# Kernel tuning notes

Measured on AMD Instinct MI355X. Metric: run time of the kernel, lower is better.

Reference implementation:

```python
import jax, jax.numpy as jnp
import numpy as np
from jax import lax

SHIFTS = (1, 2, 4, 8)

def _neighbors(x, d):
    # x: [B,C,H,W] -> [B,8,C,H,W], 8 reflection-padded directional shifts
    H, W = x.shape[2], x.shape[3]
    def p(t, l, b, r):
        return jnp.pad(x, ((0, 0), (0, 0), (t, b), (l, r)), mode='reflect')
    x0 = p(d, d, 0, 0)[:, :, :H, :W]
    x1 = p(d, 0, 0, 0)[:, :, :H, :]
    x2 = p(d, 0, 0, d)[:, :, :H, d:]
    x3 = p(0, d, 0, 0)[:, :, :, :W]
    x4 = p(0, 0, 0, d)[:, :, :, d:]
    x5 = p(0, d, d, 0)[:, :, d:, :W]
    x6 = p(0, 0, d, 0)[:, :, d:, :]
    x7 = p(0, 0, d, d)[:, :, d:, d:]
    return jnp.stack([x0, x1, x2, x3, x4, x5, x6, x7], axis=1)

def _l2norm(x):
    # F.normalize(dim=-1): x / max(||x||, 1e-12)
    n = jnp.sqrt(jnp.sum(x * x, axis=-1, keepdims=True))
    return x / jnp.maximum(n, 1e-12)

def _forward(cen, q_w, k_w, v_w, sur_w1, sur_b1, sur_w2, sur_b2, sum_weights, out_w, bn_gamma, bn_beta):
    B, C, H, W = cen.shape
    nh = len(SHIFTS)
    keys, qrys, vals = [], [], []
    for i, d in enumerate(SHIFTS):
        nb = _neighbors(cen, d)  # [B,8,C,H,W]
        w2 = jax.nn.softmax(sum_weights[i])  # [2]
        h1 = lax.conv_general_dilated(cen, sur_w1[i], (1, 1), ((d, d), (d, d)),
                                      rhs_dilation=(d, d),
                                      dimension_numbers=('NCHW', 'OIHW', 'NCHW'))
        h1 = jax.nn.relu(h1 + sur_b1[i][None, :, None, None])
        sw = jax.nn.softmax(jnp.einsum('bchw,oc->bohw', h1, sur_w2[i]) + sur_b2[i][None, :, None, None], axis=1) * w2[0]  # [B,8,H,W]
        sum_x = jnp.einsum('bkchw,bkhw->bchw', nb, sw) + cen * w2[1]
        cen_x = nb.mean(axis=1) * w2[0] + cen * w2[1]
        sur = (nb - sum_x[:, None]).reshape(B, 8 * C, H, W)  # cat of x_k - sum_x
        keys.append(jnp.einsum('bchw,oc->bohw', sur, k_w[i]))    # [B,8*hid,H,W]
        vals.append(jnp.einsum('bchw,oc->bohw', sur, v_w[i]))
        qrys.append(jnp.einsum('bchw,oc->bohw', cen_x, q_w[i]))  # [B,hid,H,W]
    HW = H * W
    # torch.stack(dim=2).view(b, nh, -1, HW): row-major reinterpretation
    K = jnp.stack(keys, axis=2).reshape(B, nh, -1, HW)
    Q = jnp.stack(qrys, axis=2).reshape(B, nh, -1, HW)
    V = jnp.stack(vals, axis=2).reshape(B, nh, -1, HW)
    K = _l2norm(K)
    Q = _l2norm(Q)
    score = jnp.einsum('bnqs,bnks->bnqk', Q, K) / np.float32(np.sqrt(HW))
    # InstanceNorm2d(nh), affine=False: normalize over last two dims per (b, head)
    mu = score.mean(axis=(-2, -1), keepdims=True)
    var = score.var(axis=(-2, -1), keepdims=True)
    score = (score - mu) * lax.rsqrt(var + 1e-5)
    attn = jax.nn.softmax(score, axis=-1)
    out = jnp.einsum('bnqk,bnks->bnqs', attn, V).reshape(B, -1, H, W)  # [B,tra,H,W]
    y = jnp.einsum('bchw,oc->bohw', out, out_w)
    # BatchNorm2d in training mode (batch statistics)
    m = y.mean(axis=(0, 2, 3), keepdims=True)
    v = y.var(axis=(0, 2, 3), keepdims=True)
    y = (y - m) * lax.rsqrt(v + 1e-5) * bn_gamma[None, :, None, None] + bn_beta[None, :, None, None]
    return jax.nn.relu(y)

def setup_inputs() -> dict:
    key = jax.random.key(0)
    ks = jax.random.split(key, 12)
    B, C, H, W = 2, 32, 128, 128
    nh, hid, tra, oc = 4, 64, 256, 256
    r = lambda k, s, sc: jax.random.normal(k, s, dtype=jnp.float32) * sc
    return {
        'cen': r(ks[0], (B, C, H, W), 1.0),
        'q_w': r(ks[1], (nh, hid, C), 0.05),
        'k_w': r(ks[2], (nh, 8 * hid, 8 * C), 0.05),
        'v_w': r(ks[3], (nh, 8 * hid, 8 * C), 0.05),
        'sur_w1': r(ks[4], (nh, C, C, 3, 3), 0.05),
        'sur_b1': r(ks[5], (nh, C), 0.02),
        'sur_w2': r(ks[6], (nh, 8, C), 0.05),
        'sur_b2': r(ks[7], (nh, 8), 0.02),
        'sum_weights': r(ks[8], (nh, 2), 0.1),
        'out_w': r(ks[9], (oc, tra), 0.05),
        'bn_gamma': jnp.ones((oc,), jnp.float32) + r(ks[10], (oc,), 0.05),
        'bn_beta': r(ks[11], (oc,), 0.05),
    }

def reference(cen, q_w, k_w, v_w, sur_w1, sur_b1, sur_w2, sur_b2, sum_weights, out_w, bn_gamma, bn_beta):
    return _forward(cen, q_w, k_w, v_w, sur_w1, sur_b1, sur_w2, sur_b2, sum_weights, out_w, bn_gamma, bn_beta)
```

## Files before the change

### kernel.cpp

```cpp
#include <hip/hip_runtime.h>


#define HW 16384
typedef unsigned short u16;
typedef unsigned int u32;
typedef __attribute__((ext_vector_type(8))) short short8;
typedef __attribute__((ext_vector_type(4))) float f32x4;

#define S_CEN 0
#define S_QW 1048576
#define S_KW 1056768
#define S_VW 1581056
#define S_W1 2105344
#define S_B1 2142208
#define S_W2 2142336
#define S_B2 2143360
#define S_SW 2143392
#define S_OW 2143400
#define S_GAMMA 2208936
#define S_BETA 2209192
#define S_TOTAL 2209456

#define G_D1 0
#define G_D2 16384
#define G_S 147456
#define G_SZ 409600

#define GP_SLOT 344064

__device__ __forceinline__ float b2f(u16 u) { return __uint_as_float(((u32)u) << 16); }
__device__ __forceinline__ u16 f2b(float f) {
  u32 u = __float_as_uint(f);
  return (u16)((u + 0x7FFFu + ((u >> 16) & 1u)) >> 16);
}
__device__ __forceinline__ float wave_sum(float v) {
  #pragma unroll
  for (int off = 32; off > 0; off >>= 1) v += __shfl_xor(v, off, 64);
  return v;
}
__device__ __forceinline__ float wave_max(float v) {
  #pragma unroll
  for (int off = 32; off > 0; off >>= 1) v = fmaxf(v, __shfl_xor(v, off, 64));
  return v;
}
__device__ __forceinline__ void unpack8(uint4 v, float* f) {
  f[0] = __uint_as_float(v.x << 16); f[1] = __uint_as_float(v.x & 0xFFFF0000u);
  f[2] = __uint_as_float(v.y << 16); f[3] = __uint_as_float(v.y & 0xFFFF0000u);
  f[4] = __uint_as_float(v.z << 16); f[5] = __uint_as_float(v.z & 0xFFFF0000u);
  f[6] = __uint_as_float(v.w << 16); f[7] = __uint_as_float(v.w & 0xFFFF0000u);
}
__device__ __forceinline__ void gload16(const u16* g, u16* l) {
  __builtin_amdgcn_global_load_lds(
      (const __attribute__((address_space(1))) void*)g,
      (__attribute__((address_space(3))) void*)l, 16, 0, 0);
}

__device__ __forceinline__ void tile_decode(int tile, int& r0, int& c0,
                                            size_t& goff, int& gstride) {
  if (tile == 0) { r0 = 0; c0 = 0; goff = G_D1; gstride = 128; }
  else if (tile < 9) { r0 = 0; c0 = 128 * tile; goff = G_D2 + (size_t)(tile - 1) * 128; gstride = 1024; }
  else if (tile < 17) {
    int t2 = tile - 9; int j = t2 >> 1, p = t2 & 1;
    r0 = 128 + 256 * j + 128 * p; c0 = r0;
    goff = G_S + (size_t)j * 65536 + (size_t)p * (128 * 256 + 128); gstride = 256;
  } else {
    int j = tile - 17;
    r0 = 128 + 256 * j; c0 = r0 + 128;
    goff = G_S + (size_t)j * 65536 + 128; gstride = 256;
  }
}

__global__ void probe(const u32* __restrict__ g, int* __restrict__ flag) {
  if (threadIdx.x == 0) {
    int ok = 1;
    #pragma unroll
    for (int i = 0; i < 4; i++) {
      u32 w = g[i];
      u32 lo = w & 0xFFFFu, hi = w >> 16;
      ok &= (lo >= 0x3E00u && lo <= 0x4100u) ? 1 : 0;
      ok &= (hi >= 0x3E00u && hi <= 0x4100u) ? 1 : 0;
    }
    *flag = ok ? 0 : 1;
  }
}

__global__ __launch_bounds__(256) void convert_all(
    const void* p0, const void* p1, const void* p2, const void* p3,
    const void* p4, const void* p5, const void* p6, const void* p7,
    const void* p8, const void* p9, const void* p10, const void* p11,
    u16* __restrict__ S, const int* __restrict__ flag) {
  const void* src; int n; int off;
  switch (blockIdx.z) {
    case 0:  src = p0;  n = 1048576; off = S_CEN; break;
    case 1:  src = p1;  n = 8192;    off = S_QW; break;
    case 2:  src = p2;  n = 524288;  off = S_KW; break;
    case 3:  src = p3;  n = 524288;  off = S_VW; break;
    case 4:  src = p4;  n = 36864;   off = S_W1; break;
    case 5:  src = p5;  n = 128;     off = S_B1; break;
    case 6:  src = p6;  n = 1024;    off = S_W2; break;
    case 7:  src = p7;  n = 32;      off = S_B2; break;
    case 8:  src = p8;  n = 8;       off = S_SW; break;
    case 9:  src = p9;  n = 65536;   off = S_OW; break;
    case 10: src = p10; n = 256;     off = S_GAMMA; break;
    default: src = p11; n = 256;     off = S_BETA; break;
  }
  int idx = (blockIdx.x * 256 + threadIdx.x) * 4;
  if (idx >= n) return;
  u16* dst = S + off + idx;
  if (*flag) {
    float4 v = ((const float4*)src)[idx >> 2];
    dst[0] = f2b(v.x); dst[1] = f2b(v.y); dst[2] = f2b(v.z); dst[3] = f2b(v.w);
  } else {
    *(ushort4*)dst = ((const ushort4*)src)[idx >> 2];
  }
}

__global__ __launch_bounds__(256) void sur_w(
    const u16* __restrict__ cen, const u16* __restrict__ w1g,
    const u16* __restrict__ b1g, const u16* __restrict__ w2g,
    float* __restrict__ lgbuf) {
  const int z = blockIdx.y;
  const int b = z >> 2, si = z & 3, d = 1 << si;
  __shared__ float w1s[9][32][32];
  __shared__ float w2s[8][32];
  __shared__ float b1s[32];
  const int t = threadIdx.x;
  for (int e = t; e < 9216; e += 256) {
    int tap = e >> 10, rem = e & 1023, ci = rem >> 5, co = rem & 31;
    w1s[tap][ci][co] = b2f(w1g[si * 9216 + co * 288 + ci * 9 + tap]);
  }
  w2s[t >> 5][t & 31] = b2f(w2g[si * 256 + t]);
  if (t < 32) b1s[t] = b2f(b1g[si * 32 + t]);
  __syncthreads();

  const int px = t >> 1;
  const int half = t & 1;
  const int ch = half * 16;
  const int hh = blockIdx.x;
  const int s = hh * 128 + px;
  const u16* cb = cen + (size_t)b * 32 * HW + (size_t)ch * HW;

  float h1[32];
  #pragma unroll
  for (int i = 0; i < 32; i++) h1[i] = 0.f;
  for (int tap = 0; tap < 9; tap++) {
    int ky = tap / 3, kx = tap - ky * 3;
    int y = hh + (ky - 1) * d, x = px + (kx - 1) * d;
    bool valid = (y >= 0 && y < 128 && x >= 0 && x < 128);
    int yc = y < 0 ? 0 : (y > 127 ? 127 : y);
    int xc = x < 0 ? 0 : (x > 127 ? 127 : x);
    int off = yc * 128 + xc;
    float vb[16];
    #pragma unroll
    for (int ci = 0; ci < 16; ci++) vb[ci] = b2f(cb[(size_t)ci * HW + off]);
    #pragma unroll
    for (int ci = 0; ci < 16; ci++) {
      float v = valid ? vb[ci] : 0.f;
      #pragma unroll
      for (int i = 0; i < 32; i++) h1[i] = fmaf(v, w1s[tap][ch + ci][i], h1[i]);
    }
  }
  #pragma unroll
  for (int i = 0; i < 32; i++) h1[i] += __shfl_xor(h1[i], 1, 64);
  #pragma unroll
  for (int i = 0; i < 32; i++) h1[i] = fmaxf(h1[i] + b1s[i], 0.f);

  float lp[4];
  #pragma unroll
  for (int k = 0; k < 4; k++) lp[k] = 0.f;
  #pragma unroll
  for (int i = 0; i < 32; i++) {
    float v = h1[i];
    #pragma unroll
    for (int k = 0; k < 4; k++) lp[k] = fmaf(v, w2s[half * 4 + k][i], lp[k]);
  }
  float* dst = lgbuf + ((size_t)z * HW + s) * 8 + half * 4;
  *(float4*)dst = make_float4(lp[0], lp[1], lp[2], lp[3]);
}

__global__ __launch_bounds__(256) void sur_scatter(
    const u16* __restrict__ cen, const float* __restrict__ lgbuf,
    const u16* __restrict__ b2g, const u16* __restrict__ swg,
    u16* __restrict__ Mbuf) {
  const int z = blockIdx.z;
  const int b = z >> 2, si = z & 3, d = 1 << si;
  const int c0 = blockIdx.y * 8;
  const int t = threadIdx.x;
  const int s = (blockIdx.x * 256 + t) * 2;
  const int h = s >> 7, w = s & 127;

  float s0 = b2f(swg[si * 2 + 0]), s1 = b2f(swg[si * 2 + 1]);
  float mx = fmaxf(s0, s1);
  float e0 = expf(s0 - mx), e1 = expf(s1 - mx);
  float w20 = e0 / (e0 + e1), w21 = e1 / (e0 + e1);

  float b2s[8];
  #pragma unroll
  for (int k = 0; k < 8; k++) b2s[k] = b2f(b2g[si * 8 + k]);

  const float* lpa = lgbuf + ((size_t)z * HW + s) * 8;
  float lga[8], lgb[8];
  {
    float4 a0 = *(const float4*)lpa,       a1 = *(const float4*)(lpa + 4);
    float4 g0 = *(const float4*)(lpa + 8), g1 = *(const float4*)(lpa + 12);
    lga[0] = a0.x; lga[1] = a0.y; lga[2] = a0.z; lga[3] = a0.w;
    lga[4] = a1.x; lga[5] = a1.y; lga[6] = a1.z; lga[7] = a1.w;
    lgb[0] = g0.x; lgb[1] = g0.y; lgb[2] = g0.z; lgb[3] = g0.w;
    lgb[4] = g1.x; lgb[5] = g1.y; lgb[6] = g1.z; lgb[7] = g1.w;
  }
  {
    #pragma unroll
    for (int k = 0; k < 8; k++) lga[k] += b2s[k];
    float lm = lga[0];
    #pragma unroll
    for (int k = 1; k < 8; k++) lm = fmaxf(lm, lga[k]);
    float ls = 0.f;
    #pragma unroll
    for (int k = 0; k < 8; k++) { lga[k] = expf(lga[k] - lm); ls += lga[k]; }
    float inv = w20 / ls;
    #pragma unroll
    for (int k = 0; k < 8; k++) lga[k] *= inv;
  }
  {
    #pragma unroll
    for (int k = 0; k < 8; k++) lgb[k] += b2s[k];
    float lm = lgb[0];
    #pragma unroll
    for (int k = 1; k < 8; k++) lm = fmaxf(lm, lgb[k]);
    float ls = 0.f;
    #pragma unroll
    for (int k = 0; k < 8; k++) { lgb[k] = expf(lgb[k] - lm); ls += lgb[k]; }
    float inv = w20 / ls;
    #pragma unroll
    for (int k = 0; k < 8; k++) lgb[k] *= inv;
  }

  const int dy[8] = {-d, -d, -d, 0, 0, d, d, d};
  const int dx[8] = {-d, 0, d, -d, d, -d, 0, d};
  int offa[8], offb[8];
  #pragma unroll
  for (int k = 0; k < 8; k++) {
    int y = h + dy[k]; y = y < 0 ? -y : (y > 127 ? 254 - y : y);
    int xa = w + dx[k]; xa = xa < 0 ? -xa : (xa > 127 ? 254 - xa : xa);
    int xb = w + 1 + dx[k]; xb = xb < 0 ? -xb : (xb > 127 ? 254 - xb : xb);
    offa[k] = y * 128 + xa;
    offb[k] = y * 128 + xb;
  }
  const u16* cb = cen + (size_t)b * 32 * HW;
  u16* Mb = Mbuf + (size_t)b * 1152 * HW;
  for (int c = c0; c < c0 + 8; c++) {
    const u16* cc = cb + (size_t)c * HW;
    u32 cvp = *(const u32*)&cc[s];
    float cva = __uint_as_float(cvp << 16), cvb = __uint_as_float(cvp & 0xFFFF0000u);
    float nba[8], nbb[8];
    #pragma unroll
    for (int k = 0; k < 8; k++) { nba[k] = b2f(cc[offa[k]]); nbb[k] = b2f(cc[offb[k]]); }
    float sxa = 0.f, mna = 0.f, sxb = 0.f, mnb = 0.f;
    #pragma unroll
    for (int k = 0; k < 8; k++) {
      sxa = fmaf(lga[k], nba[k], sxa); mna += nba[k];
      sxb = fmaf(lgb[k], nbb[k], sxb); mnb += nbb[k];
    }
    float suma = sxa + cva * w21, sumb = sxb + cvb * w21;
    u32 cx = (u32)f2b(mna * 0.125f * w20 + cva * w21) |
             ((u32)f2b(mnb * 0.125f * w20 + cvb * w21) << 16);
    *(u32*)&Mb[(size_t)(32 * si + c) * HW + s] = cx;
    #pragma unroll
    for (int k = 0; k < 8; k++) {
      u32 pk = (u32)f2b(nba[k] - suma) | ((u32)f2b(nbb[k] - sumb) << 16);
      *(u32*)&Mb[(size_t)(128 + 256 * si + k * 32 + c) * HW + s] = pk;
    }
  }
}

__global__ __launch_bounds__(256) void gram_mfma(
    const u16* __restrict__ Mbuf, float* __restrict__ Gpart) {
  const int id = blockIdx.x;
  const int tile = id >> 5, combo = id & 31;
  const int ks = combo >> 1, b = combo & 1;
  int r0, c0, gstride; size_t goff;
  tile_decode(tile, r0, c0, goff, gstride);
  const bool diag = (r0 == c0);
  const u16* Mb = Mbuf + (size_t)b * 1152 * HW;
  __shared__ u16 As[128 * 64];
  __shared__ u16 Bs[128 * 64];
  const int t = threadIdx.x;
  const int lane = t & 63, w = t >> 6;
  const int wr = w >> 1, wc = w & 1;
  const int m = lane & 15, quad = lane >> 4;
  const int lr = lane >> 3;
  const int lsl = ((lane & 7) ^ (lr & 7)) * 8;
  const int kbase = ks * 1024;
  f32x4 acc[4][4];
  #pragma unroll
  for (int i = 0; i < 4; i++)
    #pragma unroll
    for (int j = 0; j < 4; j++) acc[i][j] = (f32x4){0.f, 0.f, 0.f, 0.f};

  for (int s0 = kbase; s0 < kbase + 1024; s0 += 64) {
    #pragma unroll
    for (int q = 0; q < 4; q++) {
      const int R0 = w * 32 + q * 8;
      gload16(Mb + (size_t)(r0 + R0 + lr) * HW + s0 + lsl, &As[R0 * 64]);
    }
    if (!diag) {
      #pragma unroll
      for (int q = 0; q < 4; q++) {
        const int R0 = w * 32 + q * 8;
        gload16(Mb + (size_t)(c0 + R0 + lr) * HW + s0 + lsl, &Bs[R0 * 64]);
      }
    }
    __syncthreads();
    const u16* Bb = diag ? As : Bs;
    #pragma unroll
    for (int kh = 0; kh < 2; kh++) {
      short8 af[4], bf[4];
      const int slot = ((quad + 4 * kh) ^ (m & 7)) * 8;
      #pragma unroll
      for (int i = 0; i < 4; i++)
        af[i] = *(const short8*)&As[(wr * 64 + i * 16 + m) * 64 + slot];
      #pragma unroll
      for (int j = 0; j < 4; j++)
        bf[j] = *(const short8*)&Bb[(wc * 64 + j * 16 + m) * 64 + slot];
      #pragma unroll
      for (int i = 0; i < 4; i++)
        #pragma unroll
        for (int j = 0; j < 4; j++)
          acc[i][j] = __builtin_amdgcn_mfma_f32_16x16x32_bf16(af[i], bf[j], acc[i][j], 0, 0, 0);
    }
    __syncthreads();
  }
  float* Gb = Gpart + (size_t)(b * 16 + ks) * GP_SLOT + (size_t)tile * 16384;
  #pragma unroll
  for (int i = 0; i < 4; i++)
    #pragma unroll
    for (int j = 0; j < 4; j++) {
      int col = wc * 64 + j * 16 + m;
      #pragma unroll
      for (int r = 0; r < 4; r++) {
        int row = wr * 64 + i * 16 + quad * 4 + r;
        Gb[row * 128 + col] = acc[i][j][r];
      }
    }
}

__global__ __launch_bounds__(256) void greduce(
    const float* __restrict__ Gpart, float* __restrict__ G) {
  const int chunk = blockIdx.x, tile = blockIdx.y, b = blockIdx.z;
  int r0, c0, gstride; size_t goff;
  tile_decode(tile, r0, c0, goff, gstride);
  const int t = threadIdx.x;
  const int e = chunk * 1024 + t * 4;
  const float* base = Gpart + (size_t)b * 16 * GP_SLOT + (size_t)tile * 16384 + e;
  f32x4 acc = *(const f32x4*)base;
  #pragma unroll
  for (int s = 1; s < 16; s++) acc += *(const f32x4*)(base + (size_t)s * GP_SLOT);
  const int row = e >> 7, col = e & 127;
  *(f32x4*)&G[(size_t)b * G_SZ + goff + (size_t)row * gstride + col] = acc;
}

__global__ __launch_bounds__(256) void mirror_S(float* __restrict__ G) {
  const int j = blockIdx.x & 3, b = blockIdx.x >> 2;
  float* base = G + (size_t)b * G_SZ + G_S + (size_t)j * 65536;
  const int t = threadIdx.x;
  for (int e = t; e < 16384; e += 256) {
    int rr = e >> 7, cc = e & 127;
    base[(size_t)(128 + rr) * 256 + cc] = base[(size_t)cc * 256 + 128 + rr];
  }
}

__global__ __launch_bounds__(64) void qnorm(
    const u16* __restrict__ qw, const float* __restrict__ G,
    float* __restrict__ invQ) {
  const int bn = blockIdx.x, b = bn >> 2, n = bn & 3;
  const int rq = threadIdx.x;
  const int i = rq & 3, q1r = rq >> 2;
  const u16* qr = qw + ((size_t)(i * 64) + 16 * n + q1r) * 32;
  float v[32];
  #pragma unroll
  for (int c = 0; c < 32; c++) v[c] = b2f(qr[c]);
  const float* D1 = G + (size_t)b * G_SZ;
  float ss = 0.f;
  for (int c = 0; c < 32; c++) {
    float tmp = 0.f;
    #pragma unroll
    for (int c2 = 0; c2 < 32; c2++) tmp = fmaf(v[c2], D1[(size_t)(32 * i + c2) * 128 + 32 * i + c], tmp);
    ss = fmaf(tmp, v[c], ss);
  }
  invQ[bn * 64 + rq] = 1.f / fmaxf(sqrtf(fmaxf(ss, 0.f)), 1e-12f);
}

__global__ __launch_bounds__(256) void knorm(
    const u16* __restrict__ kw, const float* __restrict__ G,
    float* __restrict__ invK) {
  const int jj = blockIdx.x;
  const int j = jj & 3, kkg = jj >> 2;
  const int n = blockIdx.y, b = blockIdx.z;
  const int t = threadIdx.x;
  __shared__ float vs[8][256];
  for (int e = t; e < 2048; e += 256) {
    int r = e >> 8, c = e & 255;
    vs[r][c] = b2f(kw[((size_t)(j * 512) + 128 * n + kkg * 8 + r) * 256 + c]);
  }
  __syncthreads();
  const float* S = G + (size_t)b * G_SZ + G_S + (size_t)j * 65536;
  float acc[8];
  #pragma unroll
  for (int r = 0; r < 8; r++) acc[r] = 0.f;
  for (int c2 = 0; c2 < 256; c2++) {
    float sv = S[(size_t)c2 * 256 + t];
    #pragma unroll
    for (int r = 0; r < 8; r++) acc[r] = fmaf(vs[r][c2], sv, acc[r]);
  }
  #pragma unroll
  for (int r = 0; r < 8; r++) acc[r] *= vs[r][t];
  __shared__ float red[8][4];
  const int wv = t >> 6, lane = t & 63;
  #pragma unroll
  for (int r = 0; r < 8; r++) {
    float v = wave_sum(acc[r]);
    if (lane == 0) red[r][wv] = v;
  }
  __syncthreads();
  if (t < 8) {
    float tot = fmaxf(red[t][0] + red[t][1] + red[t][2] + red[t][3], 0.f);
    invK[(size_t)(b * 4 + n) * 512 + 4 * (kkg * 8 + t) + j] =
        1.f / fmaxf(sqrtf(tot), 1e-12f);
  }
}

__global__ __launch_bounds__(256) void score2(
    const u16* __restrict__ qw, const u16* __restrict__ kw,
    const float* __restrict__ G, const float* __restrict__ invQ,
    const float* __restrict__ invK, float* __restrict__ score,
    float* __restrict__ sstat) {
  const int jj = blockIdx.x;
  const int j = jj >> 1, half = jj & 1;
  const int n = blockIdx.y, b = blockIdx.z;
  const float* D2 = G + (size_t)b * G_SZ + G_D2;
  const u16* kwb = kw + ((size_t)(j * 512) + 128 * n + half * 64) * 256;
  __shared__ float As[64][132];
  __shared__ u16 Bs[64][68];
  __shared__ float KD[128][68];
  __shared__ float qws[64][32];
  const int t = threadIdx.x;
  const int tx = t & 7, ty = t >> 3;
  float acc[4][8];
  #pragma unroll
  for (int i = 0; i < 4; i++)
    #pragma unroll
    for (int u = 0; u < 8; u++) acc[i][u] = 0.f;
  for (int ch0 = 0; ch0 < 256; ch0 += 64) {
    for (int e = t; e < 8192; e += 256) {
      int r = e >> 6, kc = e & 63;
      As[kc][r] = D2[(size_t)r * 1024 + j * 256 + ch0 + kc];
    }
    for (int e = t; e < 4096; e += 256) {
      int r = e >> 6, kc = e & 63;
      Bs[kc][r] = kwb[(size_t)r * 256 + ch0 + kc];
    }
    __syncthreads();
    #pragma unroll 4
    for (int kc = 0; kc < 64; kc++) {
      float a[4];
      #pragma unroll
      for (int i = 0; i < 4; i++) a[i] = As[kc][ty * 4 + i];
      float bb[8];
      #pragma unroll
      for (int u = 0; u < 8; u++) bb[u] = b2f(Bs[kc][tx * 8 + u]);
      #pragma unroll
      for (int i = 0; i < 4; i++)
        #pragma unroll
        for (int u = 0; u < 8; u++) acc[i][u] = fmaf(a[i], bb[u], acc[i][u]);
    }
    __syncthreads();
  }
  #pragma unroll
  for (int i = 0; i < 4; i++)
    #pragma unroll
    for (int u = 0; u < 8; u++) KD[ty * 4 + i][tx * 8 + u] = acc[i][u];
  for (int e = t; e < 2048; e += 256) {
    int q = e >> 5, c = e & 31;
    int i = q & 3, q1r = q >> 2;
    qws[q][c] = b2f(qw[((size_t)(i * 64) + 16 * n + q1r) * 32 + c]);
  }
  __syncthreads();
  const int bn = b * 4 + n;
  float* sb = score + (size_t)bn * 64 * 512;
  const float* iQ = invQ + bn * 64;
  const float* iK = invK + (size_t)bn * 512;
  const float isc = 1.f / 128.f;
  float lsum = 0.f, lss = 0.f;
  for (int e = t; e < 4096; e += 256) {
    int q = e >> 6, kkl = e & 63;
    int i = q & 3;
    float s = 0.f;
    #pragma unroll
    for (int c = 0; c < 32; c++) s = fmaf(qws[q][c], KD[i * 32 + c][kkl], s);
    int col = 4 * (half * 64 + kkl) + j;
    float v = s * iQ[q] * iK[col] * isc;
    sb[(size_t)q * 512 + col] = v;
    lsum += v; lss += v * v;
  }
  lsum = wave_sum(lsum); lss = wave_sum(lss);
  __shared__ float redp[8];
  if ((t & 63) == 0) { redp[t >> 6] = lsum; redp[4 + (t >> 6)] = lss; }
  __syncthreads();
  if (t == 0) {
    atomicAdd(&sstat[bn * 2],     redp[0] + redp[1] + redp[2] + redp[3]);
    atomicAdd(&sstat[bn * 2 + 1], redp[4] + redp[5] + redp[6] + redp[7]);
  }
}

__global__ __launch_bounds__(256) void in_softmax(
    float* __restrict__ score, const float* __restrict__ sstat) {
  const int bn = blockIdx.y, rg = blockIdx.x;
  float* sb = score + (size_t)bn * 64 * 512;
  const int t = threadIdx.x;
  float mean = sstat[bn * 2] * (1.f / 32768.f);
  float var = sstat[bn * 2 + 1] * (1.f / 32768.f) - mean * mean;
  float istd = rsqrtf(var + 1e-5f);
  const int wv = t >> 6, lane = t & 63;
  for (int rr = wv; rr < 8; rr += 4) {
    int r = rg * 8 + rr;
    float z[8];
    float m = -1e30f;
    #pragma unroll
    for (int jx = 0; jx < 8; jx++) {
      z[jx] = (sb[(size_t)r * 512 + lane + 64 * jx] - mean) * istd;
      m = fmaxf(m, z[jx]);
    }
    m = wave_max(m);
    float sloc = 0.f;
    #pragma unroll
    for (int jx = 0; jx < 8; jx++) { z[jx] = expf(z[jx] - m); sloc += z[jx]; }
    sloc = wave_sum(sloc);
    float rinv = 1.f / sloc;
    #pragma unroll
    for (int jx = 0; jx < 8; jx++) sb[(size_t)r * 512 + lane + 64 * jx] = z[jx] * rinv;
  }
}

__global__ __launch_bounds__(256) void attnW2(
    const float* __restrict__ attn, const u16* __restrict__ vw,
    float* __restrict__ W2) {
  const int j = blockIdx.x >> 2, n = blockIdx.x & 3;
  const int q0 = blockIdx.y * 8, b = blockIdx.z, bn = b * 4 + n;
  const float* ab = attn + (size_t)bn * 64 * 512;
  const int t = threadIdx.x;
  __shared__ float at_s[8][128];
  for (int e = t; e < 1024; e += 256) {
    int qg = e >> 7, kk = e & 127;
    at_s[qg][kk] = ab[(size_t)(q0 + qg) * 512 + 4 * kk + j];
  }
  __syncthreads();
  float acc[8];
  #pragma unroll
  for (int qg = 0; qg < 8; qg++) acc[qg] = 0.f;
  const u16* vcol = vw + ((size_t)(j * 512) + 128 * n) * 256 + t;
  for (int kk = 0; kk < 128; kk++) {
    float v = b2f(vcol[(size_t)kk * 256]);
    #pragma unroll
    for (int qg = 0; qg < 8; qg++) acc[qg] = fmaf(at_s[qg][kk], v, acc[qg]);
  }
  #pragma unroll
  for (int qg = 0; qg < 8; qg++)
    W2[((size_t)bn * 64 + q0 + qg) * 1024 + j * 256 + t] = acc[qg];
}

__global__ __launch_bounds__(256) void wfin_k(
    const u16* __restrict__ ow, const float* __restrict__ W2,
    u16* __restrict__ Wfin16) {
  const int jc = blockIdx.x, b = blockIdx.y;
  __shared__ float col[256];
  const int t = threadIdx.x;
  col[t] = W2[((size_t)b * 256 + t) * 1024 + jc];
  __syncthreads();
  float acc = 0.f;
  const u16* owr = ow + (size_t)t * 256;
  for (int c = 0; c < 256; c++) acc = fmaf(b2f(owr[c]), col[c], acc);
  Wfin16[((size_t)b * 256 + t) * 1024 + jc] = f2b(acc);
}

__global__ __launch_bounds__(256) void y_gemm_mfma(
    const u16* __restrict__ Wfin16, const u16* __restrict__ Mbuf,
    u16* __restrict__ ybuf) {
  const int b = blockIdx.y, col0 = blockIdx.x * 64;
  __shared__ u16 As[2][256 * 64];
  __shared__ u16 Bs[2][64 * 64];
  const u16* Ab = Wfin16 + (size_t)b * 256 * 1024;
  const u16* Mb = Mbuf + (size_t)b * 1152 * HW + (size_t)128 * HW;
  const int t = threadIdx.x;
  const int lane = t & 63, w = t >> 6;
  const int m = lane & 15, quad = lane >> 4;
  const int kp = t >> 3, cs = t & 7;
  const int lr = lane >> 3;
  const int lsl = ((lane & 7) ^ (lr & 7)) * 8;
  f32x4 acc[4][4];
  #pragma unroll
  for (int i = 0; i < 4; i++)
    #pragma unroll
    for (int j = 0; j < 4; j++) acc[i][j] = (f32x4){0.f, 0.f, 0.f, 0.f};

  uint4 v0, v1;
  auto stageA = [&](int buf, int k0c) {
    #pragma unroll
    for (int q = 0; q < 8; q++)
      gload16(&Ab[(size_t)(w * 64 + q * 8 + lr) * 1024 + k0c + lsl],
              &As[buf][(w * 64 + q * 8) * 64]);
  };
  auto loadB = [&](int k0c) {
    v0 = *(const uint4*)&Mb[(size_t)(k0c + 2 * kp) * HW + col0 + cs * 8];
    v1 = *(const uint4*)&Mb[(size_t)(k0c + 2 * kp + 1) * HW + col0 + cs * 8];
  };
  auto writeB = [&](int buf) {
    u16 t0[8], t1[8];
    *(uint4*)t0 = v0; *(uint4*)t1 = v1;
    const int ksl = kp >> 2, kin = (2 * kp) & 7;
    #pragma unroll
    for (int uu = 0; uu < 8; uu++) {
      int u = (uu + t) & 7;
      int r = cs * 8 + u;
      u32 pair = (u32)t0[u] | ((u32)t1[u] << 16);
      *(u32*)&Bs[buf][r * 64 + ((ksl ^ (r & 7)) << 3) + kin] = pair;
    }
  };

  stageA(0, 0);
  loadB(0);
  writeB(0);
  __syncthreads();

  int cur = 0;
  for (int step = 0; step < 16; step++) {
    const int nxt = cur ^ 1;
    if (step < 15) {
      stageA(nxt, (step + 1) * 64);
      loadB((step + 1) * 64);
    }
    #pragma unroll
    for (int kh = 0; kh < 2; kh++) {
      short8 af[4], bf[4];
      const int slot = ((4 * kh + quad) ^ (m & 7)) * 8;
      #pragma unroll
      for (int i = 0; i < 4; i++)
        af[i] = *(const short8*)&As[cur][(w * 64 + i * 16 + m) * 64 + slot];
      #pragma unroll
      for (int j = 0; j < 4; j++)
        bf[j] = *(const short8*)&Bs[cur][(j * 16 + m) * 64 + slot];
      #pragma unroll
      for (int i = 0; i < 4; i++)
        #pragma unroll
        for (int j = 0; j < 4; j++)
          acc[i][j] = __builtin_amdgcn_mfma_f32_16x16x32_bf16(af[i], bf[j], acc[i][j], 0, 0, 0);
    }
    if (step < 15) {
      writeB(nxt);
      __syncthreads();
      cur = nxt;
    }
  }
  #pragma unroll
  for (int i = 0; i < 4; i++)
    #pragma unroll
    for (int j = 0; j < 4; j++) {
      int col = col0 + j * 16 + m;
      #pragma unroll
      for (int r = 0; r < 4; r++) {
        int row = w * 64 + i * 16 + quad * 4 + r;
        ybuf[((size_t)b * 256 + row) * HW + col] = f2b(acc[i][j][r]);
      }
    }
}

__global__ __launch_bounds__(256) void bn_stats(
    const u16* __restrict__ y, float* __restrict__ st) {
  const int o = blockIdx.x;
  const int t = threadIdx.x;
  float sum = 0.f, ss = 0.f;
  for (int bb = 0; bb < 2; bb++) {
    const u16* p = y + ((size_t)bb * 256 + o) * HW;
    for (int e = t; e < HW / 8; e += 256) {
      uint4 v = ((const uint4*)p)[e];
      float f[8];
      unpack8(v, f);
      #pragma unroll
      for (int k = 0; k < 8; k++) { sum += f[k]; ss += f[k] * f[k]; }
    }
  }
  __shared__ float red[8];
  sum = wave_sum(sum); ss = wave_sum(ss);
  if ((t & 63) == 0) { red[t >> 6] = sum; red[4 + (t >> 6)] = ss; }
  __syncthreads();
  if (t == 0) {
    float mean = (red[0] + red[1] + red[2] + red[3]) / 32768.f;
    float var = (red[4] + red[5] + red[6] + red[7]) / 32768.f - mean * mean;
    st[o * 2] = mean;
    st[o * 2 + 1] = rsqrtf(var + 1e-5f);
  }
}

__global__ __launch_bounds__(256) void bn_apply(
    const u16* __restrict__ y, const float* __restrict__ st,
    const u16* __restrict__ gamma, const u16* __restrict__ beta,
    const int* __restrict__ flag, void* __restrict__ out) {
  const int idx8 = blockIdx.x * 256 + threadIdx.x;
  const int r = idx8 >> 11;
  const int o = r & 255;
  float mean = st[o * 2], istd = st[o * 2 + 1];
  float g = b2f(gamma[o]), be = b2f(beta[o]);
  uint4 v = ((const uint4*)y)[idx8];
  float f[8];
  unpack8(v, f);
  float rr[8];
  #pragma unroll
  for (int k = 0; k < 8; k++) rr[k] = fmaxf((f[k] - mean) * istd * g + be, 0.f);
  if (*flag) {
    float* of = (float*)out + (size_t)idx8 * 8;
    *(float4*)of = make_float4(rr[0], rr[1], rr[2], rr[3]);
    *(float4*)(of + 4) = make_float4(rr[4], rr[5], rr[6], rr[7]);
  } else {
    u32 p0 = (u32)f2b(rr[0]) | ((u32)f2b(rr[1]) << 16);
    u32 p1 = (u32)f2b(rr[2]) | ((u32)f2b(rr[3]) << 16);
    u32 p2 = (u32)f2b(rr[4]) | ((u32)f2b(rr[5]) << 16);
    u32 p3 = (u32)f2b(rr[6]) | ((u32)f2b(rr[7]) << 16);
    ((uint4*)out)[idx8] = make_uint4(p0, p1, p2, p3);
  }
}

extern "C" void kernel_launch(void* const* d_in, const int* in_sizes, int n_in,
                              void* d_out, int out_size, void* d_ws, size_t ws_size,
                              hipStream_t stream) {
  float* G     = (float*)d_ws;
  float* score = G + 819200;
  float* invQ  = score + 262144;
  float* invK  = invQ + 512;
  float* W2    = invK + 4096;
  float* Wfin  = W2 + 524288;
  float* bnst  = Wfin + 524288;
  float* sstat = bnst + 512;
  int* flag    = (int*)(sstat + 16);
  u16* Sbuf    = (u16*)(flag + 16);
  u16* Mbuf    = Sbuf + S_TOTAL;
  u16* ybuf    = Mbuf + 37748736;
  u16* Wfin16  = (u16*)Wfin;
  float* lgbuf = (float*)ybuf;
  float* Gpart = (float*)ybuf;

  probe<<<1, 64, 0, stream>>>((const u32*)d_in[10], flag);
  convert_all<<<dim3(1024, 1, 12), 256, 0, stream>>>(
      d_in[0], d_in[1], d_in[2], d_in[3], d_in[4], d_in[5], d_in[6], d_in[7],
      d_in[8], d_in[9], d_in[10], d_in[11], Sbuf, flag);

  sur_w<<<dim3(128, 8), 256, 0, stream>>>(
      Sbuf + S_CEN, Sbuf + S_W1, Sbuf + S_B1, Sbuf + S_W2, lgbuf);
  sur_scatter<<<dim3(32, 4, 8), 256, 0, stream>>>(
      Sbuf + S_CEN, lgbuf, Sbuf + S_B2, Sbuf + S_SW, Mbuf);
  hipMemsetAsync(sstat, 0, 16 * sizeof(float), stream);
  gram_mfma<<<672, 256, 0, stream>>>(Mbuf, Gpart);
  greduce<<<dim3(16, 21, 2), 256, 0, stream>>>(Gpart, G);
  mirror_S<<<8, 256, 0, stream>>>(G);
  qnorm<<<8, 64, 0, stream>>>(Sbuf + S_QW, G, invQ);
  knorm<<<dim3(64, 4, 2), 256, 0, stream>>>(Sbuf + S_KW, G, invK);
  score2<<<dim3(8, 4, 2), 256, 0, stream>>>(
      Sbuf + S_QW, Sbuf + S_KW, G, invQ, invK, score, sstat);
  in_softmax<<<dim3(8, 8), 256, 0, stream>>>(score, sstat);
  attnW2<<<dim3(16, 8, 2), 256, 0, stream>>>(score, Sbuf + S_VW, W2);
  wfin_k<<<dim3(1024, 2), 256, 0, stream>>>(Sbuf + S_OW, W2, Wfin16);
  y_gemm_mfma<<<dim3(256, 2), 256, 0, stream>>>(Wfin16, Mbuf, ybuf);
  bn_stats<<<256, 256, 0, stream>>>(ybuf, bnst);
  bn_apply<<<4096, 256, 0, stream>>>(ybuf, bnst, Sbuf + S_GAMMA, Sbuf + S_BETA,
                                     flag, d_out);
}
```

Measured before the change: 425.0 us.

## Compute dilated 3x3 surround conv with bf16 MFMA on channel-last transposed input

Adds a transpose kernel that writes cen in pixel-major, channel-last layout, then rewrites sur_w to stage each tap's input rows into shared memory and run the 32x32 per-tap products with 16x16x32 bf16 MFMA instead of scalar FMAs. Weights stay bf16 in a swizzled shared layout. Out-of-range taps are skipped per row, or read zeros from a zero buffer per pixel. h1 is staged through shared memory for the final 8-way projection. This removes a large scalar FMA loop and strided per-channel global loads, at the cost of an extra kernel launch, a transpose pass and more barriers.

```diff
diff --git a/kernel.cpp b/kernel.cpp
--- a/kernel.cpp
+++ b/kernel.cpp
@@ -115,66 +115,115 @@
   }
 }
 
+__global__ __launch_bounds__(256) void transp(
+    const u16* __restrict__ cen, u16* __restrict__ cenT) {
+  __shared__ u16 tile[32][258];
+  const int t = threadIdx.x;
+  const int s0 = blockIdx.x * 256;
+  const u16* cb = cen + (size_t)blockIdx.y * 32 * HW;
+  for (int e = t; e < 2048; e += 256) {
+    int ci = e >> 6, sx = (e & 63) * 4;
+    *(u32*)&tile[ci][sx] = *(const u32*)&cb[(size_t)ci * HW + s0 + sx];
+    *(u32*)&tile[ci][sx + 2] = *(const u32*)&cb[(size_t)ci * HW + s0 + sx + 2];
+  }
+  __syncthreads();
+  u16* ob = cenT + (size_t)blockIdx.y * HW * 32;
+  for (int e = t; e < 1024; e += 256) {
+    int px = e >> 2, cg = (e & 3) * 8;
+    u16 tmp[8];
+    #pragma unroll
+    for (int k = 0; k < 8; k++) tmp[k] = tile[cg + k][px];
+    *(uint4*)&ob[(size_t)(s0 + px) * 32 + cg] = *(uint4*)tmp;
+  }
+}
+
 __global__ __launch_bounds__(256) void sur_w(
-    const u16* __restrict__ cen, const u16* __restrict__ w1g,
+    const u16* __restrict__ cenT, const u16* __restrict__ w1g,
     const u16* __restrict__ b1g, const u16* __restrict__ w2g,
-    float* __restrict__ lgbuf) {
+    const u16* __restrict__ zbuf, float* __restrict__ lgbuf) {
   const int z = blockIdx.y;
   const int b = z >> 2, si = z & 3, d = 1 << si;
-  __shared__ float w1s[9][32][32];
+  const int hh = blockIdx.x;
+  __shared__ __align__(16) char smem[27776];
+  u16* Bs = (u16*)smem;
+  u16* w1s = (u16*)(smem + 8192);
+  float* h1s = (float*)smem;
   __shared__ float w2s[8][32];
   __shared__ float b1s[32];
   const int t = threadIdx.x;
   for (int e = t; e < 9216; e += 256) {
-    int tap = e >> 10, rem = e & 1023, ci = rem >> 5, co = rem & 31;
-    w1s[tap][ci][co] = b2f(w1g[si * 9216 + co * 288 + ci * 9 + tap]);
+    int tap = e >> 10, rem = e & 1023, co = rem >> 5, ci = rem & 31;
+    int dst = tap * 1024 + co * 32 + ((((ci >> 3) ^ (co & 3)) << 3) | (ci & 7));
+    w1s[dst] = w1g[si * 9216 + co * 288 + ci * 9 + tap];
   }
   w2s[t >> 5][t & 31] = b2f(w2g[si * 256 + t]);
   if (t < 32) b1s[t] = b2f(b1g[si * 32 + t]);
-  __syncthreads();
-
-  const int px = t >> 1;
-  const int half = t & 1;
-  const int ch = half * 16;
-  const int hh = blockIdx.x;
-  const int s = hh * 128 + px;
-  const u16* cb = cen + (size_t)b * 32 * HW + (size_t)ch * HW;
-
-  float h1[32];
-  #pragma unroll
-  for (int i = 0; i < 32; i++) h1[i] = 0.f;
+
+  const u16* cb = cenT + (size_t)b * HW * 32;
+  const int lane = t & 63, w = t >> 6;
+  const int m = lane & 15, quad = lane >> 4;
+  const int slot8 = (quad ^ (m & 3)) << 3;
+  f32x4 acc[2][2];
+  #pragma unroll
+  for (int i = 0; i < 2; i++)
+    #pragma unroll
+    for (int j = 0; j < 2; j++) acc[i][j] = (f32x4){0.f, 0.f, 0.f, 0.f};
+
   for (int tap = 0; tap < 9; tap++) {
-    int ky = tap / 3, kx = tap - ky * 3;
-    int y = hh + (ky - 1) * d, x = px + (kx - 1) * d;
-    bool valid = (y >= 0 && y < 128 && x >= 0 && x < 128);
-    int yc = y < 0 ? 0 : (y > 127 ? 127 : y);
-    int xc = x < 0 ? 0 : (x > 127 ? 127 : x);
-    int off = yc * 128 + xc;
-    float vb[16];
-    #pragma unroll
-    for (int ci = 0; ci < 16; ci++) vb[ci] = b2f(cb[(size_t)ci * HW + off]);
-    #pragma unroll
-    for (int ci = 0; ci < 16; ci++) {
-      float v = valid ? vb[ci] : 0.f;
-      #pragma unroll
-      for (int i = 0; i < 32; i++) h1[i] = fmaf(v, w1s[tap][ch + ci][i], h1[i]);
-    }
-  }
-  #pragma unroll
-  for (int i = 0; i < 32; i++) h1[i] += __shfl_xor(h1[i], 1, 64);
-  #pragma unroll
-  for (int i = 0; i < 32; i++) h1[i] = fmaxf(h1[i] + b1s[i], 0.f);
-
+    const int ky = tap / 3, kx = tap - ky * 3;
+    const int y = hh + (ky - 1) * d;
+    if (y < 0 || y > 127) continue;
+    const int dx = (kx - 1) * d;
+    #pragma unroll
+    for (int q = 0; q < 2; q++) {
+      const int e = q * 256 + t;
+      const int px = e >> 2, ck = e & 3;
+      const int x = px + dx;
+      const u16* src = ((unsigned)x < 128u)
+          ? cb + ((size_t)(y * 128 + x) * 32 + ((ck ^ (px & 3)) << 3))
+          : zbuf;
+      gload16(src, Bs + (size_t)e * 8);
+    }
+    __syncthreads();
+    short8 af[2], bf[2];
+    #pragma unroll
+    for (int i = 0; i < 2; i++)
+      af[i] = *(const short8*)&Bs[(w * 32 + i * 16 + m) * 32 + slot8];
+    #pragma unroll
+    for (int j = 0; j < 2; j++)
+      bf[j] = *(const short8*)&w1s[tap * 1024 + (j * 16 + m) * 32 + slot8];
+    #pragma unroll
+    for (int i = 0; i < 2; i++)
+      #pragma unroll
+      for (int j = 0; j < 2; j++)
+        acc[i][j] = __builtin_amdgcn_mfma_f32_16x16x32_bf16(af[i], bf[j], acc[i][j], 0, 0, 0);
+    __syncthreads();
+  }
+
+  #pragma unroll
+  for (int i = 0; i < 2; i++)
+    #pragma unroll
+    for (int j = 0; j < 2; j++) {
+      const int co = j * 16 + m;
+      #pragma unroll
+      for (int r = 0; r < 4; r++) {
+        const int px = w * 32 + i * 16 + quad * 4 + r;
+        h1s[px * 33 + co] = fmaxf(acc[i][j][r] + b1s[co], 0.f);
+      }
+    }
+  __syncthreads();
+
+  const int px = t >> 1, half = t & 1;
   float lp[4];
   #pragma unroll
   for (int k = 0; k < 4; k++) lp[k] = 0.f;
   #pragma unroll
   for (int i = 0; i < 32; i++) {
-    float v = h1[i];
+    const float v = h1s[px * 33 + i];
     #pragma unroll
     for (int k = 0; k < 4; k++) lp[k] = fmaf(v, w2s[half * 4 + k][i], lp[k]);
   }
-  float* dst = lgbuf + ((size_t)z * HW + s) * 8 + half * 4;
+  float* dst = lgbuf + ((size_t)z * HW + hh * 128 + px) * 8 + half * 4;
   *(float4*)dst = make_float4(lp[0], lp[1], lp[2], lp[3]);
 }
 
@@ -739,24 +788,27 @@
   float* Wfin  = W2 + 524288;
   float* bnst  = Wfin + 524288;
   float* sstat = bnst + 512;
-  int* flag    = (int*)(sstat + 16);
+  float* zbuf  = sstat + 16;
+  int* flag    = (int*)(zbuf + 16);
   u16* Sbuf    = (u16*)(flag + 16);
   u16* Mbuf    = Sbuf + S_TOTAL;
   u16* ybuf    = Mbuf + 37748736;
   u16* Wfin16  = (u16*)Wfin;
   float* lgbuf = (float*)ybuf;
+  u16* cenT    = (u16*)(lgbuf + 1048576);
   float* Gpart = (float*)ybuf;
 
   probe<<<1, 64, 0, stream>>>((const u32*)d_in[10], flag);
   convert_all<<<dim3(1024, 1, 12), 256, 0, stream>>>(
       d_in[0], d_in[1], d_in[2], d_in[3], d_in[4], d_in[5], d_in[6], d_in[7],
       d_in[8], d_in[9], d_in[10], d_in[11], Sbuf, flag);
-
+  hipMemsetAsync(sstat, 0, 32 * sizeof(float), stream);
+
+  transp<<<dim3(64, 2), 256, 0, stream>>>(Sbuf + S_CEN, cenT);
   sur_w<<<dim3(128, 8), 256, 0, stream>>>(
-      Sbuf + S_CEN, Sbuf + S_W1, Sbuf + S_B1, Sbuf + S_W2, lgbuf);
+      cenT, Sbuf + S_W1, Sbuf + S_B1, Sbuf + S_W2, (const u16*)zbuf, lgbuf);
   sur_scatter<<<dim3(32, 4, 8), 256, 0, stream>>>(
       Sbuf + S_CEN, lgbuf, Sbuf + S_B2, Sbuf + S_SW, Mbuf);
-  hipMemsetAsync(sstat, 0, 16 * sizeof(float), stream);
   gram_mfma<<<672, 256, 0, stream>>>(Mbuf, Gpart);
   greduce<<<dim3(16, 21, 2), 256, 0, stream>>>(Gpart, G);
   mirror_S<<<8, 256, 0, stream>>>(G);
```

Result: faster. 363.6 us (-14.4%).
